# Performance work log

Measured on AMD Instinct MI355X. Metric: run time of the kernel, lower is better.

The kernel has to match this reference:

```python
import jax, jax.numpy as jnp
from jax import lax
import numpy as np

DN = ('NCHW', 'OIHW', 'NCHW')


def bilinear_grid_sample(x, grid):
    """F.grid_sample(x, grid) with mode='bilinear', padding_mode='zeros', align_corners=False.
    x: [N,C,H,W], grid: [N,Hg,Wg,2] with grid[...,0]=x(width) coord, grid[...,1]=y(height)."""
    N, C, H, W = x.shape
    gx, gy = grid[..., 0], grid[..., 1]
    ix = ((gx + 1.0) * W - 1.0) * 0.5  # unnormalize (align_corners=False)
    iy = ((gy + 1.0) * H - 1.0) * 0.5
    x0 = jnp.floor(ix); y0 = jnp.floor(iy)
    x1 = x0 + 1.0;      y1 = y0 + 1.0
    x_nhwc = jnp.transpose(x, (0, 2, 3, 1))  # [N,H,W,C]
    b = jnp.arange(N)[:, None, None]

    def gather(xi, yi):
        valid = (xi >= 0) & (xi <= W - 1) & (yi >= 0) & (yi <= H - 1)
        xc = jnp.clip(xi, 0, W - 1).astype(jnp.int32)
        yc = jnp.clip(yi, 0, H - 1).astype(jnp.int32)
        return x_nhwc[b, yc, xc] * valid[..., None].astype(x.dtype)  # [N,Hg,Wg,C]

    wa = ((x1 - ix) * (y1 - iy))[..., None]
    wb = ((x1 - ix) * (iy - y0))[..., None]
    wc = ((ix - x0) * (y1 - iy))[..., None]
    wd = ((ix - x0) * (iy - y0))[..., None]
    out = (gather(x0, y0) * wa + gather(x0, y1) * wb
           + gather(x1, y0) * wc + gather(x1, y1) * wd)
    return jnp.transpose(out, (0, 3, 1, 2))  # [N,C,Hg,Wg]


def setup_inputs() -> dict:
    key = jax.random.key(0)
    k1, k2, k3, k4 = jax.random.split(key, 4)
    N, C, H, W, Cout = 8, 64, 256, 256, 64
    x = jax.random.normal(k1, (N, C, H, W), dtype=jnp.float32)
    # original zero-inits conv_deform; use tiny random weights so offsets are small but non-trivial
    w_def = jax.random.normal(k2, (2, C, 5, 5), dtype=jnp.float32) * 0.01
    b_def = jnp.zeros((2,), dtype=jnp.float32)
    w_conv = jax.random.normal(k3, (Cout, C, 3, 3), dtype=jnp.float32) * (1.0 / np.sqrt(C * 9))
    b_conv = jax.random.normal(k4, (Cout,), dtype=jnp.float32) * 0.01
    return {"x": x, "w_def": w_def, "b_def": b_def, "w_conv": w_conv, "b_conv": b_conv}


def reference(x, w_def, b_def, w_conv, b_conv):
    N, C, H, W = x.shape
    # offset branch: conv2d(in->2, k=5, pad=2), to NHWC
    off = lax.conv_general_dilated(x, w_def, (1, 1), [(2, 2), (2, 2)], dimension_numbers=DN)
    off = jnp.transpose(off, (0, 2, 3, 1)) + b_def  # [N,H,W,2]
    # regular grid: meshgrid(ij) of linspace over H then W, cat[xx,yy]
    xx, yy = jnp.meshgrid(jnp.linspace(-1.0, 1.0, H), jnp.linspace(-1.0, 1.0, W), indexing='ij')
    grid = off + jnp.stack([xx, yy], axis=-1)[None].astype(x.dtype)
    xs = bilinear_grid_sample(x, grid)
    out = lax.conv_general_dilated(xs, w_conv, (1, 1), [(1, 1), (1, 1)], dimension_numbers=DN)
    return out + b_conv[None, :, None, None]
```

## Files before the change

### kernel.cpp

```cpp
#include <hip/hip_runtime.h>

typedef unsigned int u32;
typedef __attribute__((ext_vector_type(8))) short short8;
typedef __attribute__((ext_vector_type(4))) float f32x4;

__device__ __forceinline__ unsigned short f2bf(float f){
  u32 u = __builtin_bit_cast(u32, f);
  u = u + 0x7fffu + ((u >> 16) & 1u);
  return (unsigned short)(u >> 16);
}
__device__ __forceinline__ float bf2f(unsigned short h){
  return __builtin_bit_cast(float, ((u32)h) << 16);
}

__global__ __launch_bounds__(256) void k_pack_b(const float* __restrict__ w_conv,
                                                unsigned short* __restrict__ Bp){
  int idx = blockIdx.x*256 + threadIdx.x;
  if (idx >= 9*2*4*64*8) return;
  int i    = idx & 7;
  int lane = (idx >> 3) & 63;
  int t    = (idx >> 9) & 3;
  int chunk= (idx >> 11) & 1;
  int tap  = idx >> 12;
  int co = t*16 + (lane & 15);
  int c  = chunk*32 + (lane >> 4)*8 + i;
  int ki = tap/3, kj = tap%3;
  Bp[idx] = f2bf(w_conv[((co*64 + c)*3 + ki)*3 + kj]);
}

__global__ __launch_bounds__(256) void k_transpose(const float* __restrict__ x,
                                                   unsigned short* __restrict__ xn){
  __shared__ float tile[64][65];
  int n = blockIdx.y, pix0 = blockIdx.x*64;
  int tid = threadIdx.x, lane = tid & 63, grp = tid >> 6;
  #pragma unroll
  for (int k = 0; k < 16; k++){
    int c = k*4 + grp;
    tile[c][lane] = x[(n*64 + c)*65536 + pix0 + lane];
  }
  __syncthreads();
  #pragma unroll
  for (int k = 0; k < 16; k++){
    int p = k*4 + grp;
    xn[(n*65536 + pix0 + p)*64 + lane] = f2bf(tile[lane][p]);
  }
}

__global__ __launch_bounds__(256) void k_offset(const float* __restrict__ x,
                                                const float* __restrict__ w_def,
                                                const float* __restrict__ b_def,
                                                float2* __restrict__ gridc){
  __shared__ float red[4][4][2][256];
  int b = blockIdx.x;
  int xcd  = b & 7;
  int w8   = b >> 3;
  int qloc = w8 & 7;
  int n    = w8 >> 3;
  int i0   = (xcd*8 + qloc)*4;
  int tid = threadIdx.x, l = tid & 63;
  int wv = __builtin_amdgcn_readfirstlane(tid >> 6);

  float me0 = (l == 0)  ? 0.f : 1.f;
  float me1 = (l == 63) ? 0.f : 1.f;
  int o0 = (l == 0)  ? 0 : -2;
  int o3 = (l == 63) ? 2 : 4;

  float a0[4][4], a1[4][4];
  #pragma unroll
  for (int s = 0; s < 4; s++)
    #pragma unroll
    for (int q = 0; q < 4; q++){ a0[s][q] = 0.f; a1[s][q] = 0.f; }

  for (int cc = 0; cc < 16; cc++){
    int c = (wv << 4) + cc;
    const float* rp  = x + ((n << 6) + c)*65536 + (l << 2);
    const float* wq0 = w_def + c*25;
    const float* wq1 = w_def + 1600 + c*25;
    float w0[25], w1[25];
    #pragma unroll
    for (int t = 0; t < 25; t++){ w0[t] = wq0[t]; w1[t] = wq1[t]; }

    #pragma unroll
    for (int r = 0; r < 8; r++){
      int gi = i0 - 2 + r;
      if (gi < 0 || gi > 255) continue;
      const float* rr = rp + (gi << 8);
      float2 d0 = *(const float2*)(rr + o0);
      float2 d1 = *(const float2*)(rr);
      float2 d2 = *(const float2*)(rr + 2);
      float2 d3 = *(const float2*)(rr + o3);
      float wd[8];
      wd[0] = d0.x * me0; wd[1] = d0.y * me0;
      wd[2] = d1.x;       wd[3] = d1.y;
      wd[4] = d2.x;       wd[5] = d2.y;
      wd[6] = d3.x * me1; wd[7] = d3.y * me1;
      #pragma unroll
      for (int s = 0; s < 4; s++){
        int ki = r - s;
        if (ki < 0 || ki > 4) continue;
        #pragma unroll
        for (int q = 0; q < 4; q++)
          #pragma unroll
          for (int kj = 0; kj < 5; kj++){
            a0[s][q] = fmaf(wd[q+kj], w0[ki*5+kj], a0[s][q]);
            a1[s][q] = fmaf(wd[q+kj], w1[ki*5+kj], a1[s][q]);
          }
      }
    }
  }

  #pragma unroll
  for (int s = 0; s < 4; s++)
    #pragma unroll
    for (int q = 0; q < 4; q++){
      red[wv][s][0][(l << 2) + q] = a0[s][q];
      red[wv][s][1][(l << 2) + q] = a1[s][q];
    }
  __syncthreads();

  float bd0 = b_def[0], bd1 = b_def[1];
  #pragma unroll
  for (int v = 0; v < 4; v++){
    int p = tid + (v << 8);
    int s = p >> 8, col = p & 255;
    float s0 = red[0][s][0][col] + red[1][s][0][col] + red[2][s][0][col] + red[3][s][0][col];
    float s1 = red[0][s][1][col] + red[1][s][1][col] + red[2][s][1][col] + red[3][s][1][col];
    int i = i0 + s;
    float gx = s0 + bd0 + (-1.0f + (2.0f/255.0f)*(float)i);
    float gy = s1 + bd1 + (-1.0f + (2.0f/255.0f)*(float)col);
    float ix = ((gx + 1.0f)*256.0f - 1.0f)*0.5f;
    float iy = ((gy + 1.0f)*256.0f - 1.0f)*0.5f;
    gridc[((n << 8) + i)*256 + col] = make_float2(ix, iy);
  }
}

__global__ __launch_bounds__(256) void k_sample(const unsigned short* __restrict__ xn,
                                                const float2* __restrict__ gridc,
                                                unsigned short* __restrict__ xs){
  int n = blockIdx.z, i0 = blockIdx.y*16, j0 = blockIdx.x*16;
  int tid = threadIdx.x, w = tid >> 6, lane = tid & 63;
  for (int s = 0; s < 4; s++){
    int i = i0 + w*4 + s;
    int rowbase = (n<<16) + (i<<8);
    #pragma unroll 2
    for (int j1 = 0; j1 < 16; j1++){
      int j = j0 + j1;
      float2 g = gridc[rowbase + j];
      float ix = g.x, iy = g.y;
      float x0f = floorf(ix), y0f = floorf(iy);
      float fx = ix - x0f, fy = iy - y0f;
      int x0 = (int)x0f, y0 = (int)y0f;
      int x1 = x0 + 1, y1 = y0 + 1;
      float m00 = ((x0>=0)&(x0<256)&(y0>=0)&(y0<256)) ? 1.f : 0.f;
      float m01 = ((x0>=0)&(x0<256)&(y1>=0)&(y1<256)) ? 1.f : 0.f;
      float m10 = ((x1>=0)&(x1<256)&(y0>=0)&(y0<256)) ? 1.f : 0.f;
      float m11 = ((x1>=0)&(x1<256)&(y1>=0)&(y1<256)) ? 1.f : 0.f;
      int x0c = x0 < 0 ? 0 : (x0 > 255 ? 255 : x0);
      int x1c = x1 < 0 ? 0 : (x1 > 255 ? 255 : x1);
      int y0c = y0 < 0 ? 0 : (y0 > 255 ? 255 : y0);
      int y1c = y1 < 0 ? 0 : (y1 > 255 ? 255 : y1);
      int nb = (n<<16);
      float v00 = bf2f(xn[((nb + (y0c<<8) + x0c)<<6) + lane]) * m00;
      float v01 = bf2f(xn[((nb + (y1c<<8) + x0c)<<6) + lane]) * m01;
      float v10 = bf2f(xn[((nb + (y0c<<8) + x1c)<<6) + lane]) * m10;
      float v11 = bf2f(xn[((nb + (y1c<<8) + x1c)<<6) + lane]) * m11;
      float r = (1.f-fx)*((1.f-fy)*v00 + fy*v01) + fx*((1.f-fy)*v10 + fy*v11);
      xs[((rowbase + j)<<6) + lane] = f2bf(r);
    }
  }
}

__global__ __launch_bounds__(256,2) void k_conv2(const unsigned short* __restrict__ xs,
                                                 const unsigned short* __restrict__ Bp,
                                                 const float* __restrict__ b_conv,
                                                 float* __restrict__ out){
  __shared__ unsigned char Al[324*128];
  __shared__ unsigned char Bl[24576];
  int n = blockIdx.z, i0 = blockIdx.y*16, j0 = blockIdx.x*16;
  int tid = threadIdx.x, w = tid >> 6, l = tid & 63;

  const uint4* xs4 = (const uint4*)xs;
  for (int u = tid; u < 324*8; u += 256){
    int p = u >> 3, q = u & 7;
    int rr = p/18, cc = p%18;
    int gi = i0 - 1 + rr, gj = j0 - 1 + cc;
    uint4 v = make_uint4(0u,0u,0u,0u);
    if (gi >= 0 && gi < 256 && gj >= 0 && gj < 256)
      v = xs4[((n<<16) + (gi<<8) + gj)*8 + q];
    int byte = (p*128 + q*16) ^ ((p & 7) << 4);
    *(uint4*)(Al + byte) = v;
  }

  f32x4 zero = {0.f,0.f,0.f,0.f};
  f32x4 acc[4][4];
  #pragma unroll
  for (int m = 0; m < 4; m++)
    #pragma unroll
    for (int t = 0; t < 4; t++) acc[m][t] = zero;

  #pragma unroll
  for (int ki = 0; ki < 3; ki++){
    __syncthreads();
    {
      const uint4* src = (const uint4*)(Bp + ki*12288);
      uint4* dst = (uint4*)Bl;
      #pragma unroll
      for (int u = 0; u < 6; u++) dst[tid + 256*u] = src[tid + 256*u];
    }
    __syncthreads();
    #pragma unroll
    for (int kj = 0; kj < 3; kj++)
      #pragma unroll
      for (int ch = 0; ch < 2; ch++){
        short8 a[4];
        #pragma unroll
        for (int m = 0; m < 4; m++){
          int p = (w*4 + m + ki)*18 + (l & 15) + kj;
          int byte = (p*128 + ch*64 + ((l >> 4) << 4)) ^ ((p & 7) << 4);
          a[m] = *(const short8*)(Al + byte);
        }
        #pragma unroll
        for (int t = 0; t < 4; t++){
          short8 b = *(const short8*)(Bl + (((kj*2 + ch)*4 + t)*64 + l)*16);
          #pragma unroll
          for (int m = 0; m < 4; m++)
            acc[m][t] = __builtin_amdgcn_mfma_f32_16x16x32_bf16(a[m], b, acc[m][t], 0, 0, 0);
        }
      }
  }

  int colp0 = (l >> 4) * 4;
  #pragma unroll
  for (int t = 0; t < 4; t++){
    int co = t*16 + (l & 15);
    float bias = b_conv[co];
    #pragma unroll
    for (int m = 0; m < 4; m++){
      int r = w*4 + m;
      f32x4 v = acc[m][t];
      v[0] += bias; v[1] += bias; v[2] += bias; v[3] += bias;
      *(f32x4*)(&out[(((n*64 + co)<<8) + i0 + r)*256 + j0 + colp0]) = v;
    }
  }
}

extern "C" void kernel_launch(void* const* d_in, const int* in_sizes, int n_in,
                              void* d_out, int out_size, void* d_ws, size_t ws_size,
                              hipStream_t stream) {
  const float* x      = (const float*)d_in[0];
  const float* w_def  = (const float*)d_in[1];
  const float* b_def  = (const float*)d_in[2];
  const float* w_conv = (const float*)d_in[3];
  const float* b_conv = (const float*)d_in[4];
  float* out = (float*)d_out;

  unsigned char* ws = (unsigned char*)d_ws;
  unsigned short* xn    = (unsigned short*)(ws);
  unsigned short* xsamp = (unsigned short*)(ws + 67108864);
  float2*         gridc = (float2*)(ws + 134217728);
  unsigned short* Bp    = (unsigned short*)(ws + 138412032);

  k_pack_b   <<<144, 256, 0, stream>>>(w_conv, Bp);
  k_transpose<<<dim3(1024, 8), 256, 0, stream>>>(x, xn);
  k_offset   <<<512, 256, 0, stream>>>(x, w_def, b_def, gridc);
  k_sample   <<<dim3(16, 16, 8), 256, 0, stream>>>(xn, gridc, xsamp);
  k_conv2    <<<dim3(16, 16, 8), 256, 0, stream>>>(xsamp, Bp, b_conv, out);
}
```

Baseline: 435.8 us.

## Fuse bilinear sampling into conv kernel and read weights directly from global

Removes the separate sampling kernel and its intermediate bf16 buffer. The conv kernel now computes the bilinear samples for its 18x18 halo tile straight into shared memory, with each thread handling four channels through vectorized loads. It also drops the shared-memory staging of the weight tile and its barriers, loading B fragments from global or L2 per MFMA step. In exchange, the halo pixels are sampled redundantly, about 27% extra gather work, and weight reads now depend on cache hits.

```diff
diff --git a/kernel.cpp b/kernel.cpp
--- a/kernel.cpp
+++ b/kernel.cpp
@@ -134,61 +134,58 @@
   }
 }
 
-__global__ __launch_bounds__(256) void k_sample(const unsigned short* __restrict__ xn,
-                                                const float2* __restrict__ gridc,
-                                                unsigned short* __restrict__ xs){
-  int n = blockIdx.z, i0 = blockIdx.y*16, j0 = blockIdx.x*16;
-  int tid = threadIdx.x, w = tid >> 6, lane = tid & 63;
-  for (int s = 0; s < 4; s++){
-    int i = i0 + w*4 + s;
-    int rowbase = (n<<16) + (i<<8);
-    #pragma unroll 2
-    for (int j1 = 0; j1 < 16; j1++){
-      int j = j0 + j1;
-      float2 g = gridc[rowbase + j];
-      float ix = g.x, iy = g.y;
-      float x0f = floorf(ix), y0f = floorf(iy);
-      float fx = ix - x0f, fy = iy - y0f;
-      int x0 = (int)x0f, y0 = (int)y0f;
-      int x1 = x0 + 1, y1 = y0 + 1;
-      float m00 = ((x0>=0)&(x0<256)&(y0>=0)&(y0<256)) ? 1.f : 0.f;
-      float m01 = ((x0>=0)&(x0<256)&(y1>=0)&(y1<256)) ? 1.f : 0.f;
-      float m10 = ((x1>=0)&(x1<256)&(y0>=0)&(y0<256)) ? 1.f : 0.f;
-      float m11 = ((x1>=0)&(x1<256)&(y1>=0)&(y1<256)) ? 1.f : 0.f;
-      int x0c = x0 < 0 ? 0 : (x0 > 255 ? 255 : x0);
-      int x1c = x1 < 0 ? 0 : (x1 > 255 ? 255 : x1);
-      int y0c = y0 < 0 ? 0 : (y0 > 255 ? 255 : y0);
-      int y1c = y1 < 0 ? 0 : (y1 > 255 ? 255 : y1);
-      int nb = (n<<16);
-      float v00 = bf2f(xn[((nb + (y0c<<8) + x0c)<<6) + lane]) * m00;
-      float v01 = bf2f(xn[((nb + (y1c<<8) + x0c)<<6) + lane]) * m01;
-      float v10 = bf2f(xn[((nb + (y0c<<8) + x1c)<<6) + lane]) * m10;
-      float v11 = bf2f(xn[((nb + (y1c<<8) + x1c)<<6) + lane]) * m11;
-      float r = (1.f-fx)*((1.f-fy)*v00 + fy*v01) + fx*((1.f-fy)*v10 + fy*v11);
-      xs[((rowbase + j)<<6) + lane] = f2bf(r);
-    }
-  }
-}
-
-__global__ __launch_bounds__(256,2) void k_conv2(const unsigned short* __restrict__ xs,
-                                                 const unsigned short* __restrict__ Bp,
-                                                 const float* __restrict__ b_conv,
-                                                 float* __restrict__ out){
+__global__ __launch_bounds__(256,2) void k_conv2s(const unsigned short* __restrict__ xn,
+                                                  const float2* __restrict__ gridc,
+                                                  const unsigned short* __restrict__ Bp,
+                                                  const float* __restrict__ b_conv,
+                                                  float* __restrict__ out){
   __shared__ unsigned char Al[324*128];
-  __shared__ unsigned char Bl[24576];
   int n = blockIdx.z, i0 = blockIdx.y*16, j0 = blockIdx.x*16;
   int tid = threadIdx.x, w = tid >> 6, l = tid & 63;
 
-  const uint4* xs4 = (const uint4*)xs;
-  for (int u = tid; u < 324*8; u += 256){
-    int p = u >> 3, q = u & 7;
-    int rr = p/18, cc = p%18;
-    int gi = i0 - 1 + rr, gj = j0 - 1 + cc;
-    uint4 v = make_uint4(0u,0u,0u,0u);
-    if (gi >= 0 && gi < 256 && gj >= 0 && gj < 256)
-      v = xs4[((n<<16) + (gi<<8) + gj)*8 + q];
-    int byte = (p*128 + q*16) ^ ((p & 7) << 4);
-    *(uint4*)(Al + byte) = v;
+  int sub   = tid & 15;
+  int pbase = tid >> 4;
+  #pragma unroll 2
+  for (int pass = 0; pass < 21; ++pass){
+    int p = pass*16 + pbase;
+    if (p < 324){
+      int rr = p/18, cc = p - rr*18;
+      int gi = i0 - 1 + rr, gj = j0 - 1 + cc;
+      u32 pk0 = 0, pk1 = 0;
+      if (gi >= 0 && gi < 256 && gj >= 0 && gj < 256){
+        float2 g = gridc[(((n << 8) + gi) << 8) + gj];
+        float ix = g.x, iy = g.y;
+        float x0f = floorf(ix), y0f = floorf(iy);
+        float fx = ix - x0f, fy = iy - y0f;
+        int x0 = (int)x0f, y0 = (int)y0f;
+        int x1 = x0 + 1, y1 = y0 + 1;
+        float m00 = ((x0>=0)&(x0<256)&(y0>=0)&(y0<256)) ? 1.f : 0.f;
+        float m01 = ((x0>=0)&(x0<256)&(y1>=0)&(y1<256)) ? 1.f : 0.f;
+        float m10 = ((x1>=0)&(x1<256)&(y0>=0)&(y0<256)) ? 1.f : 0.f;
+        float m11 = ((x1>=0)&(x1<256)&(y1>=0)&(y1<256)) ? 1.f : 0.f;
+        int x0c = x0 < 0 ? 0 : (x0 > 255 ? 255 : x0);
+        int x1c = x1 < 0 ? 0 : (x1 > 255 ? 255 : x1);
+        int y0c = y0 < 0 ? 0 : (y0 > 255 ? 255 : y0);
+        int y1c = y1 < 0 ? 0 : (y1 > 255 ? 255 : y1);
+        int nb = n << 16, s4 = sub << 2;
+        ushort4 v00 = *(const ushort4*)(xn + (((nb + (y0c<<8) + x0c) << 6) + s4));
+        ushort4 v01 = *(const ushort4*)(xn + (((nb + (y1c<<8) + x0c) << 6) + s4));
+        ushort4 v10 = *(const ushort4*)(xn + (((nb + (y0c<<8) + x1c) << 6) + s4));
+        ushort4 v11 = *(const ushort4*)(xn + (((nb + (y1c<<8) + x1c) << 6) + s4));
+        float w00 = (1.f-fx)*(1.f-fy)*m00;
+        float w01 = (1.f-fx)*fy*m01;
+        float w10 = fx*(1.f-fy)*m10;
+        float w11 = fx*fy*m11;
+        float r0 = bf2f(v00.x)*w00 + bf2f(v01.x)*w01 + bf2f(v10.x)*w10 + bf2f(v11.x)*w11;
+        float r1 = bf2f(v00.y)*w00 + bf2f(v01.y)*w01 + bf2f(v10.y)*w10 + bf2f(v11.y)*w11;
+        float r2 = bf2f(v00.z)*w00 + bf2f(v01.z)*w01 + bf2f(v10.z)*w10 + bf2f(v11.z)*w11;
+        float r3 = bf2f(v00.w)*w00 + bf2f(v01.w)*w01 + bf2f(v10.w)*w10 + bf2f(v11.w)*w11;
+        pk0 = (u32)f2bf(r0) | ((u32)f2bf(r1) << 16);
+        pk1 = (u32)f2bf(r2) | ((u32)f2bf(r3) << 16);
+      }
+      int byte = ((p << 7) + (sub << 3)) ^ ((p & 7) << 4);
+      *(uint2*)(Al + byte) = make_uint2(pk0, pk1);
+    }
   }
 
   f32x4 zero = {0.f,0.f,0.f,0.f};
@@ -198,20 +195,19 @@
     #pragma unroll
     for (int t = 0; t < 4; t++) acc[m][t] = zero;
 
-  #pragma unroll
-  for (int ki = 0; ki < 3; ki++){
-    __syncthreads();
-    {
-      const uint4* src = (const uint4*)(Bp + ki*12288);
-      uint4* dst = (uint4*)Bl;
-      #pragma unroll
-      for (int u = 0; u < 6; u++) dst[tid + 256*u] = src[tid + 256*u];
-    }
-    __syncthreads();
+  __syncthreads();
+
+  const short8* bp8 = (const short8*)Bp;
+  #pragma unroll
+  for (int ki = 0; ki < 3; ki++)
     #pragma unroll
     for (int kj = 0; kj < 3; kj++)
       #pragma unroll
       for (int ch = 0; ch < 2; ch++){
+        short8 bfr[4];
+        #pragma unroll
+        for (int t = 0; t < 4; t++)
+          bfr[t] = bp8[(((ki*3 + kj)*2 + ch)*4 + t)*64 + l];
         short8 a[4];
         #pragma unroll
         for (int m = 0; m < 4; m++){
@@ -220,14 +216,11 @@
           a[m] = *(const short8*)(Al + byte);
         }
         #pragma unroll
-        for (int t = 0; t < 4; t++){
-          short8 b = *(const short8*)(Bl + (((kj*2 + ch)*4 + t)*64 + l)*16);
+        for (int t = 0; t < 4; t++)
           #pragma unroll
           for (int m = 0; m < 4; m++)
-            acc[m][t] = __builtin_amdgcn_mfma_f32_16x16x32_bf16(a[m], b, acc[m][t], 0, 0, 0);
-        }
+            acc[m][t] = __builtin_amdgcn_mfma_f32_16x16x32_bf16(a[m], bfr[t], acc[m][t], 0, 0, 0);
       }
-  }
 
   int colp0 = (l >> 4) * 4;
   #pragma unroll
@@ -256,13 +249,11 @@
 
   unsigned char* ws = (unsigned char*)d_ws;
   unsigned short* xn    = (unsigned short*)(ws);
-  unsigned short* xsamp = (unsigned short*)(ws + 67108864);
-  float2*         gridc = (float2*)(ws + 134217728);
-  unsigned short* Bp    = (unsigned short*)(ws + 138412032);
+  float2*         gridc = (float2*)(ws + 67108864);
+  unsigned short* Bp    = (unsigned short*)(ws + 71303168);
 
   k_pack_b   <<<144, 256, 0, stream>>>(w_conv, Bp);
   k_transpose<<<dim3(1024, 8), 256, 0, stream>>>(x, xn);
   k_offset   <<<512, 256, 0, stream>>>(x, w_def, b_def, gridc);
-  k_sample   <<<dim3(16, 16, 8), 256, 0, stream>>>(xn, gridc, xsamp);
-  k_conv2    <<<dim3(16, 16, 8), 256, 0, stream>>>(xsamp, Bp, b_conv, out);
-}
+  k_conv2s   <<<dim3(16, 16, 8), 256, 0, stream>>>(xn, gridc, Bp, b_conv, out);
+}
```

Measured after the change: 415.6 us. 4.6% less time.
